# Performance work log

Hardware: AMD Instinct MI355X
Metric: run time of the kernel (lower is better)

The kernel has to match this reference:

```python
import jax, jax.numpy as jnp
import numpy as np

B, T, D = 256, 512, 64
E = 32            # station embedding dim
H = 256           # hidden size
HOR = 24          # horizon steps
STATIONS = 1000
DIN0 = D + E      # effective input dim of layer 0


def _grud_cell(x, mask, delta, x_last, h_prev, gx, gh, Wr, br, Wz, bz, Wh, bh):
    # x, mask, delta, x_last: [B, din]; h_prev: [B, H]
    x_decayed = jnp.exp(-jax.nn.relu(delta * gx)) * x_last
    x_filled = jnp.where(mask > 0, x, x_decayed)
    h_decay = jnp.exp(-jax.nn.relu(delta.mean(axis=1, keepdims=True) * gh))
    h_dec = h_decay * h_prev
    comb = jnp.concatenate([x_filled, h_dec], axis=1)
    r = jax.nn.sigmoid(comb @ Wr + br)
    z = jax.nn.sigmoid(comb @ Wz + bz)
    comb_h = jnp.concatenate([x_filled, r * h_dec], axis=1)
    h_tilde = jnp.tanh(comb_h @ Wh + bh)
    return (1.0 - z) * h_dec + z * h_tilde


def setup_inputs() -> dict:
    key = jax.random.key(0)
    ks = jax.random.split(key, 32)
    def lin(k, fan_in, fan_out):
        bound = 1.0 / np.sqrt(fan_in)
        kw, kb = jax.random.split(k)
        W = jax.random.uniform(kw, (fan_in, fan_out), jnp.float32, -bound, bound)
        b = jax.random.uniform(kb, (fan_out,), jnp.float32, -bound, bound)
        return W, b
    x = jax.random.normal(ks[0], (B, T, D), jnp.float32)
    mask = (jax.random.uniform(ks[1], (B, T, D)) < 0.8).astype(jnp.float32)
    delta = jax.random.uniform(ks[2], (B, T, D), jnp.float32)
    x_last_obs = jax.random.normal(ks[3], (B, T, D), jnp.float32)
    station_idx = jax.random.randint(ks[4], (B,), 0, STATIONS)
    emb = jax.random.normal(ks[5], (STATIONS, E), jnp.float32)
    Wr0, br0 = lin(ks[6], DIN0 + H, H)
    Wz0, bz0 = lin(ks[7], DIN0 + H, H)
    Wh0, bh0 = lin(ks[8], DIN0 + H, H)
    Wr1, br1 = lin(ks[9], H + H, H)
    Wz1, bz1 = lin(ks[10], H + H, H)
    Wh1, bh1 = lin(ks[11], H + H, H)
    Wp1, bp1 = lin(ks[12], H, H)
    Wp2, bp2 = lin(ks[13], H, HOR * 2)
    return dict(x=x, mask=mask, delta=delta, x_last_obs=x_last_obs,
                station_idx=station_idx, emb=emb,
                gx0=jnp.ones((DIN0,), jnp.float32), gh0=jnp.ones((H,), jnp.float32),
                Wr0=Wr0, br0=br0, Wz0=Wz0, bz0=bz0, Wh0=Wh0, bh0=bh0,
                gx1=jnp.ones((H,), jnp.float32), gh1=jnp.ones((H,), jnp.float32),
                Wr1=Wr1, br1=br1, Wz1=Wz1, bz1=bz1, Wh1=Wh1, bh1=bh1,
                Wp1=Wp1, bp1=bp1, Wp2=Wp2, bp2=bp2)


def reference(x, mask, delta, x_last_obs, station_idx, emb,
              gx0, gh0, Wr0, br0, Wz0, bz0, Wh0, bh0,
              gx1, gh1, Wr1, br1, Wz1, bz1, Wh1, bh1,
              Wp1, bp1, Wp2, bp2):
    e = emb[station_idx]                              # [B, E]
    e_seq = jnp.broadcast_to(e[:, None, :], (B, T, E))
    x_c = jnp.concatenate([x, e_seq], axis=-1)        # [B, T, D+E]
    xl_c = jnp.concatenate([x_last_obs, e_seq], axis=-1)
    m_c = jnp.concatenate([mask, jnp.zeros((B, T, E), x.dtype)], axis=-1)
    d_c = jnp.concatenate([delta, jnp.zeros((B, T, E), x.dtype)], axis=-1)
    # wait: torch does NOT extend mask/delta; it keeps them at input_dim? No —
    # cell expects delta shape == input_dim of the cell. In torch, mask/delta are
    # NOT concatenated, which would break shapes unless mask/delta already match.
    # Torch code passes mask[:, t, :] of width D into a cell of width D+E; torch
    # broadcasting of elementwise ops (delta * gamma_x with gamma_x width D+E)
    # would fail unless D == D+E. Faithful runnable semantics: embedding slots are
    # always 'observed' with zero delta (mask=1, delta=0, last_obs=emb).
    m_c = jnp.concatenate([mask, jnp.ones((B, T, E), x.dtype)], axis=-1)

    # time-major for scan: [T, B, *]
    xs = (jnp.swapaxes(x_c, 0, 1), jnp.swapaxes(m_c, 0, 1),
          jnp.swapaxes(d_c, 0, 1), jnp.swapaxes(xl_c, 0, 1))

    ones_h = jnp.ones((B, H), x.dtype)
    zeros_h = jnp.zeros((B, H), x.dtype)

    def step(hs, inp):
        h0, h1 = hs
        x_t, m_t, d_t, xl_t = inp
        h0 = _grud_cell(x_t, m_t, d_t, xl_t, h0, gx0, gh0, Wr0, br0, Wz0, bz0, Wh0, bh0)
        # layer 1: mask=1, delta=0, x_last = h0 (as in torch forward)
        h1 = _grud_cell(h0, ones_h, zeros_h, h0, h1, gx1, gh1, Wr1, br1, Wz1, bz1, Wh1, bh1)
        return (h0, h1), None

    (h0, h1), _ = jax.lax.scan(step, (zeros_h, zeros_h), xs)
    out = jax.nn.relu(h1 @ Wp1 + bp1) @ Wp2 + bp2     # [B, HOR*2]
    return out.reshape(B, HOR, 2)
```

## Files before the change

kernel.cpp:

```cpp
#include <hip/hip_runtime.h>
#include <hip/hip_fp16.h>


#define BB   256
#define TT   512
#define DX   64
#define EE   32
#define HH   256
#define RING 4

#define OFF_W0X_R 0
#define OFF_W0X_Z 24576
#define OFF_W0X_H 49152
#define OFF_W0H_R 73728
#define OFF_W0H_Z 139264
#define OFF_W0H_H 204800
#define OFF_W1X_R 270336
#define OFF_W1X_Z 335872
#define OFF_W1X_H 401408
#define OFF_W1H_R 466944
#define OFF_W1H_Z 532480
#define OFF_W1H_H 598016
#define PACK_TOTAL 663552

#define MSG_OFF   1327104
#define MSG_U32   768
#define FLAG_OFF  (MSG_OFF + 128*RING*MSG_U32*4)
#define CFLAG_OFF (FLAG_OFF + 128*RING*4)

typedef _Float16 half2_t __attribute__((ext_vector_type(2)));

__global__ void pack_weights(const float* __restrict__ Wr0, const float* __restrict__ Wz0,
                             const float* __restrict__ Wh0, const float* __restrict__ Wr1,
                             const float* __restrict__ Wz1, const float* __restrict__ Wh1,
                             __half* __restrict__ dst) {
  int idx = blockIdx.x * blockDim.x + threadIdx.x;
  if (idx >= PACK_TOTAL) return;
  const float* src;
  int row0, local;
  if (idx < 73728) {
    int r = idx / 24576; local = idx % 24576;
    src = (r == 0) ? Wr0 : (r == 1) ? Wz0 : Wh0;
    row0 = 0;
  } else {
    int q = (idx - 73728) / 65536; local = (idx - 73728) % 65536;
    if (q < 3)      { src = (q == 0) ? Wr0 : (q == 1) ? Wz0 : Wh0; row0 = 96;  }
    else if (q < 6) { src = (q == 3) ? Wr1 : (q == 4) ? Wz1 : Wh1; row0 = 0;   }
    else            { src = (q == 6) ? Wr1 : (q == 7) ? Wz1 : Wh1; row0 = 256; }
  }
  int seg = local >> 13;
  int rem = local & 8191;
  int j   = rem >> 5;
  int s   = (rem >> 3) & 3;
  int i   = rem & 7;
  int row = row0 + seg * 32 + s * 8 + i;
  dst[idx] = __float2half(src[(size_t)row * HH + j]);
}

__device__ __forceinline__ float dot8(uint4 w, uint4 v, float acc) {
#if __has_builtin(__builtin_amdgcn_fdot2)
  union { uint4 u; half2_t h[4]; } W, V;
  W.u = w; V.u = v;
  acc = __builtin_amdgcn_fdot2(W.h[0], V.h[0], acc, false);
  acc = __builtin_amdgcn_fdot2(W.h[1], V.h[1], acc, false);
  acc = __builtin_amdgcn_fdot2(W.h[2], V.h[2], acc, false);
  acc = __builtin_amdgcn_fdot2(W.h[3], V.h[3], acc, false);
#else
  union { unsigned u; __half2 h; } cw, cv;
  float2 wf, vf;
  cw.u = w.x; cv.u = v.x; wf = __half22float2(cw.h); vf = __half22float2(cv.h);
  acc = fmaf(wf.x, vf.x, acc); acc = fmaf(wf.y, vf.y, acc);
  cw.u = w.y; cv.u = v.y; wf = __half22float2(cw.h); vf = __half22float2(cv.h);
  acc = fmaf(wf.x, vf.x, acc); acc = fmaf(wf.y, vf.y, acc);
  cw.u = w.z; cv.u = v.z; wf = __half22float2(cw.h); vf = __half22float2(cv.h);
  acc = fmaf(wf.x, vf.x, acc); acc = fmaf(wf.y, vf.y, acc);
  cw.u = w.w; cv.u = v.w; wf = __half22float2(cw.h); vf = __half22float2(cv.h);
  acc = fmaf(wf.x, vf.x, acc); acc = fmaf(wf.y, vf.y, acc);
#endif
  return acc;
}

__device__ __forceinline__ float kred(float a) {
  a += __shfl_xor(a, 1, 64);
  a += __shfl_xor(a, 2, 64);
  return a;
}

__device__ __forceinline__ float sigm(float x) { return 1.f / (1.f + __expf(-x)); }

__device__ __forceinline__ void spin_eq(uint32_t* p, uint32_t want) {
  for (int it = 0; it < 1000000; ++it) {
    if (__hip_atomic_load(p, __ATOMIC_RELAXED, __HIP_MEMORY_SCOPE_AGENT) == want) return;
    __builtin_amdgcn_s_sleep(1);
  }
}

__global__ __launch_bounds__(1024)
__attribute__((amdgpu_waves_per_eu(4, 4)))
void grud_pipe(const float* __restrict__ x, const float* __restrict__ mask,
               const float* __restrict__ delta, const float* __restrict__ xl,
               const int* __restrict__ sidx, const float* __restrict__ emb,
               const float* __restrict__ gx0, const float* __restrict__ gh0,
               const float* __restrict__ br0, const float* __restrict__ bz0,
               const float* __restrict__ bh0, const float* __restrict__ br1,
               const float* __restrict__ bz1, const float* __restrict__ bh1,
               const float* __restrict__ Wp1, const float* __restrict__ bp1,
               const float* __restrict__ Wp2, const float* __restrict__ bp2,
               const __half* __restrict__ PW, uint32_t* wsu, float* __restrict__ out)
{
  const int bid = blockIdx.x;
  const bool isA = bid < 128;
  const int pair = isA ? bid : (bid - 128);
  const int tid = threadIdx.x;
  const int j = tid >> 2, s = tid & 3, s8 = s * 8, jb = j * 4 + s;

  uint32_t* msgbase = wsu + (MSG_OFF >> 2) + (size_t)pair * (RING * MSG_U32);
  uint32_t* flag    = wsu + (FLAG_OFF >> 2) + pair * RING;
  uint32_t* cflag   = wsu + (CFLAG_OFF >> 2) + pair * RING;

  __shared__ __align__(16) uint4  wlds[8192];
  __shared__ __align__(16) __half xfh[2][96];
  __shared__ __align__(16) __half hdech[2][256];
  __shared__ __align__(16) __half rhh[2][256];
  __shared__ __align__(16) __half h0h[2][256];
  __shared__ __align__(16) __half h0c[2][256];
  __shared__ __align__(16) __half h1h[2][256];
  __shared__ __align__(16) float  fbuf[2][256];
  __shared__ float p1f[256];
  __shared__ float sdel[2];

  if (isA) {
    const uint4* W0XR = (const uint4*)(PW + OFF_W0X_R);
    const uint4* W0XZ = (const uint4*)(PW + OFF_W0X_Z);
    const uint4* W0XH = (const uint4*)(PW + OFF_W0X_H);
    const uint4* W0HR = (const uint4*)(PW + OFF_W0H_R);
    const uint4* W0HZ = (const uint4*)(PW + OFF_W0H_Z);
    const uint4* W0HH = (const uint4*)(PW + OFF_W0H_H);
    const uint4* W1XH = (const uint4*)(PW + OFF_W1X_H);
    #pragma unroll 2
    for (int seg = 0; seg < 8; ++seg) wlds[seg * 1024 + jb] = W0HH[seg * 1024 + jb];

    const float brj0 = br0[j], bzj0 = bz0[j], bhj0 = bh0[j];
    const float gh0j = gh0[j];
    float h0j0 = 0.f, h0j1 = 0.f;
    if (tid < 512) { int g = tid >> 8, k = tid & 255; h0h[g][k] = __float2half(0.f); }
    if (tid < 64)  { int g = tid >> 5, e = tid & 31;
                     xfh[g][DX + e] = __float2half(emb[(size_t)sidx[2 * pair + g] * EE + e]); }
    float gx0k = 0.f;
    if (tid < 128) gx0k = gx0[tid & 63];
    const size_t xb0 = (size_t)(2 * pair) * TT * DX, xb1 = (size_t)(2 * pair + 1) * TT * DX;
    float xv = 0, mv = 0, dv = 0, xlv = 0;
    if (tid < 128) { size_t a = (tid < 64 ? xb0 : xb1) + (tid & 63);
                     xv = x[a]; mv = mask[a]; dv = delta[a]; xlv = xl[a]; }
    __syncthreads();

    for (int t = 0; t < TT; ++t) {
      const int slot = t & (RING - 1);
      if (tid == 0 && t >= RING) spin_eq(&cflag[slot], (uint32_t)(t - RING + 1));
      if (tid < 128) {
        int g = tid >> 6;
        float xd = __expf(-fmaxf(dv * gx0k, 0.f)) * xlv;
        xfh[g][tid & 63] = __float2half(mv > 0.f ? xv : xd);
        float ssum = dv;
        #pragma unroll
        for (int o = 32; o > 0; o >>= 1) ssum += __shfl_down(ssum, o, 64);
        if ((tid & 63) == 0) sdel[g] = ssum * (1.f / 96.f);
      }
      __syncthreads();
      float hd0 = __expf(-fmaxf(sdel[0] * gh0j, 0.f)) * h0j0;
      float hd1 = __expf(-fmaxf(sdel[1] * gh0j, 0.f)) * h0j1;
      if (s == 0) { hdech[0][j] = __float2half(hd0); hdech[1][j] = __float2half(hd1); }
      __syncthreads();
      if (tid < 128 && t + 1 < TT) {
        size_t a = (tid < 64 ? xb0 : xb1) + (size_t)(t + 1) * DX + (tid & 63);
        xv = x[a]; mv = mask[a]; dv = delta[a]; xlv = xl[a];
      }
      float ar0 = 0, ar1v = 0, az0 = 0, az1v = 0, ah0 = 0, ah1v = 0;
      #pragma unroll
      for (int seg = 0; seg < 3; ++seg) {
        uint4 v0 = *(const uint4*)(&xfh[0][seg * 32 + s8]);
        uint4 v1 = *(const uint4*)(&xfh[1][seg * 32 + s8]);
        uint4 wr = W0XR[seg * 1024 + jb], wz = W0XZ[seg * 1024 + jb], wh = W0XH[seg * 1024 + jb];
        ar0 = dot8(wr, v0, ar0); ar1v = dot8(wr, v1, ar1v);
        az0 = dot8(wz, v0, az0); az1v = dot8(wz, v1, az1v);
        ah0 = dot8(wh, v0, ah0); ah1v = dot8(wh, v1, ah1v);
      }
      #pragma unroll 2
      for (int seg = 0; seg < 8; ++seg) {
        uint4 v0 = *(const uint4*)(&hdech[0][seg * 32 + s8]);
        uint4 v1 = *(const uint4*)(&hdech[1][seg * 32 + s8]);
        uint4 wr = W0HR[seg * 1024 + jb], wz = W0HZ[seg * 1024 + jb];
        ar0 = dot8(wr, v0, ar0); ar1v = dot8(wr, v1, ar1v);
        az0 = dot8(wz, v0, az0); az1v = dot8(wz, v1, az1v);
      }
      ar0 = kred(ar0) + brj0; ar1v = kred(ar1v) + brj0;
      az0 = kred(az0) + bzj0; az1v = kred(az1v) + bzj0;
      float r0 = sigm(ar0), r1g = sigm(ar1v), z0 = sigm(az0), z1g = sigm(az1v);
      if (s == 0) { rhh[0][j] = __float2half(r0 * hd0); rhh[1][j] = __float2half(r1g * hd1); }
      __syncthreads();
      #pragma unroll 2
      for (int seg = 0; seg < 8; ++seg) {
        uint4 w  = wlds[seg * 1024 + jb];
        uint4 v0 = *(const uint4*)(&rhh[0][seg * 32 + s8]);
        uint4 v1 = *(const uint4*)(&rhh[1][seg * 32 + s8]);
        ah0 = dot8(w, v0, ah0); ah1v = dot8(w, v1, ah1v);
      }
      ah0 = kred(ah0) + bhj0; ah1v = kred(ah1v) + bhj0;
      h0j0 = (1.f - z0) * hd0 + z0 * tanhf(ah0);
      h0j1 = (1.f - z1g) * hd1 + z1g * tanhf(ah1v);
      if (s == 0) { h0h[0][j] = __float2half(h0j0); h0h[1][j] = __float2half(h0j1); }
      __syncthreads();
      float ax0 = 0.f, ax1 = 0.f;
      #pragma unroll 2
      for (int seg = 0; seg < 8; ++seg) {
        uint4 w  = W1XH[seg * 1024 + jb];
        uint4 v0 = *(const uint4*)(&h0h[0][seg * 32 + s8]);
        uint4 v1 = *(const uint4*)(&h0h[1][seg * 32 + s8]);
        ax0 = dot8(w, v0, ax0); ax1 = dot8(w, v1, ax1);
      }
      ax0 = kred(ax0); ax1 = kred(ax1);
      uint32_t* msg = msgbase + slot * MSG_U32;
      if (s == 0) {
        __hip_atomic_store(msg + 256 + j, __float_as_uint(ax0), __ATOMIC_RELAXED, __HIP_MEMORY_SCOPE_AGENT);
        __hip_atomic_store(msg + 512 + j, __float_as_uint(ax1), __ATOMIC_RELAXED, __HIP_MEMORY_SCOPE_AGENT);
      }
      if (tid < 256)
        __hip_atomic_store(msg + tid, ((const uint32_t*)h0h)[tid], __ATOMIC_RELAXED, __HIP_MEMORY_SCOPE_AGENT);
      __syncthreads();
      if (tid == 0)
        __hip_atomic_store(&flag[slot], (uint32_t)(t + 1), __ATOMIC_RELAXED, __HIP_MEMORY_SCOPE_AGENT);
    }
  } else {
    const uint4* W1XR = (const uint4*)(PW + OFF_W1X_R);
    const uint4* W1XZ = (const uint4*)(PW + OFF_W1X_Z);
    const uint4* W1HR = (const uint4*)(PW + OFF_W1H_R);
    const uint4* W1HZ = (const uint4*)(PW + OFF_W1H_Z);
    const uint4* W1HH = (const uint4*)(PW + OFF_W1H_H);
    #pragma unroll 2
    for (int seg = 0; seg < 8; ++seg) wlds[seg * 1024 + jb] = W1HH[seg * 1024 + jb];
    const float brj1 = br1[j], bzj1 = bz1[j], bhj1 = bh1[j];
    float h1j0 = 0.f, h1j1 = 0.f;
    if (tid < 512) { int g = tid >> 8, k = tid & 255; h1h[g][k] = __float2half(0.f); }
    __syncthreads();

    for (int t = 0; t < TT; ++t) {
      const int slot = t & (RING - 1);
      if (tid == 0) spin_eq(&flag[slot], (uint32_t)(t + 1));
      __syncthreads();
      uint32_t* msg = msgbase + slot * MSG_U32;
      if (tid < 256)
        ((uint32_t*)h0c)[tid] = __hip_atomic_load(msg + tid, __ATOMIC_RELAXED, __HIP_MEMORY_SCOPE_AGENT);
      else if (tid < 768) {
        int idx = tid - 256;
        fbuf[idx >> 8][idx & 255] =
            __uint_as_float(__hip_atomic_load(msg + tid, __ATOMIC_RELAXED, __HIP_MEMORY_SCOPE_AGENT));
      }
      __syncthreads();
      if (tid == 0)
        __hip_atomic_store(&cflag[slot], (uint32_t)(t + 1), __ATOMIC_RELAXED, __HIP_MEMORY_SCOPE_AGENT);
      float ar0 = 0, ar1v = 0, az0 = 0, az1v = 0;
      #pragma unroll 2
      for (int seg = 0; seg < 8; ++seg) {
        uint4 u0 = *(const uint4*)(&h0c[0][seg * 32 + s8]);
        uint4 u1 = *(const uint4*)(&h0c[1][seg * 32 + s8]);
        uint4 v0 = *(const uint4*)(&h1h[0][seg * 32 + s8]);
        uint4 v1 = *(const uint4*)(&h1h[1][seg * 32 + s8]);
        uint4 wxr = W1XR[seg * 1024 + jb], wxz = W1XZ[seg * 1024 + jb];
        uint4 whr = W1HR[seg * 1024 + jb], whz = W1HZ[seg * 1024 + jb];
        ar0 = dot8(wxr, u0, ar0);  ar0 = dot8(whr, v0, ar0);
        ar1v = dot8(wxr, u1, ar1v); ar1v = dot8(whr, v1, ar1v);
        az0 = dot8(wxz, u0, az0);  az0 = dot8(whz, v0, az0);
        az1v = dot8(wxz, u1, az1v); az1v = dot8(whz, v1, az1v);
      }
      ar0 = kred(ar0) + brj1; ar1v = kred(ar1v) + brj1;
      az0 = kred(az0) + bzj1; az1v = kred(az1v) + bzj1;
      float r0 = sigm(ar0), r1g = sigm(ar1v), z0 = sigm(az0), z1g = sigm(az1v);
      if (s == 0) { rhh[0][j] = __float2half(r0 * h1j0); rhh[1][j] = __float2half(r1g * h1j1); }
      __syncthreads();
      float p0 = 0.f, p1 = 0.f;
      #pragma unroll 2
      for (int seg = 0; seg < 8; ++seg) {
        uint4 w  = wlds[seg * 1024 + jb];
        uint4 v0 = *(const uint4*)(&rhh[0][seg * 32 + s8]);
        uint4 v1 = *(const uint4*)(&rhh[1][seg * 32 + s8]);
        p0 = dot8(w, v0, p0); p1 = dot8(w, v1, p1);
      }
      p0 = kred(p0); p1 = kred(p1);
      float ahf0 = fbuf[0][j] + p0 + bhj1;
      float ahf1 = fbuf[1][j] + p1 + bhj1;
      h1j0 = (1.f - z0) * h1j0 + z0 * tanhf(ahf0);
      h1j1 = (1.f - z1g) * h1j1 + z1g * tanhf(ahf1);
      if (s == 0) { h1h[0][j] = __float2half(h1j0); h1h[1][j] = __float2half(h1j1); }
    }

    if (s == 0) { fbuf[0][j] = h1j0; fbuf[1][j] = h1j1; }
    __syncthreads();
    for (int g = 0; g < 2; ++g) {
      float a1 = 0.f; int k0 = s * 64;
      #pragma unroll 8
      for (int k = 0; k < 64; ++k) a1 = fmaf(fbuf[g][k0 + k], Wp1[(size_t)(k0 + k) * HH + j], a1);
      a1 = kred(a1) + bp1[j];
      if (s == 0) p1f[j] = fmaxf(a1, 0.f);
      __syncthreads();
      if (tid < 192) {
        int jo = tid >> 2, so = tid & 3; float o = 0.f; int kk0 = so * 64;
        #pragma unroll 8
        for (int k = 0; k < 64; ++k) o = fmaf(p1f[kk0 + k], Wp2[(size_t)(kk0 + k) * 48 + jo], o);
        o += __shfl_xor(o, 1, 64);
        o += __shfl_xor(o, 2, 64);
        if (so == 0) out[(size_t)(2 * pair + g) * 48 + jo] = o + bp2[jo];
      }
      __syncthreads();
    }
  }
}

extern "C" void kernel_launch(void* const* d_in, const int* in_sizes, int n_in,
                              void* d_out, int out_size, void* d_ws, size_t ws_size,
                              hipStream_t stream) {
  const float* x    = (const float*)d_in[0];
  const float* mask = (const float*)d_in[1];
  const float* delta= (const float*)d_in[2];
  const float* xl   = (const float*)d_in[3];
  const int*   sidx = (const int*)d_in[4];
  const float* emb  = (const float*)d_in[5];
  const float* gx0  = (const float*)d_in[6];
  const float* gh0  = (const float*)d_in[7];
  const float* Wr0  = (const float*)d_in[8];
  const float* br0  = (const float*)d_in[9];
  const float* Wz0  = (const float*)d_in[10];
  const float* bz0  = (const float*)d_in[11];
  const float* Wh0  = (const float*)d_in[12];
  const float* bh0  = (const float*)d_in[13];
  const float* Wr1  = (const float*)d_in[16];
  const float* br1  = (const float*)d_in[17];
  const float* Wz1  = (const float*)d_in[18];
  const float* bz1  = (const float*)d_in[19];
  const float* Wh1  = (const float*)d_in[20];
  const float* bh1  = (const float*)d_in[21];
  const float* Wp1  = (const float*)d_in[22];
  const float* bp1  = (const float*)d_in[23];
  const float* Wp2  = (const float*)d_in[24];
  const float* bp2  = (const float*)d_in[25];
  __half*   PW  = (__half*)d_ws;
  uint32_t* wsu = (uint32_t*)d_ws;
  float* out = (float*)d_out;

  hipLaunchKernelGGL(pack_weights, dim3((PACK_TOTAL + 255) / 256), dim3(256), 0, stream,
                     Wr0, Wz0, Wh0, Wr1, Wz1, Wh1, PW);
  hipLaunchKernelGGL(grud_pipe, dim3(BB), dim3(1024), 0, stream,
                     x, mask, delta, xl, sidx, emb, gx0, gh0,
                     br0, bz0, bh0, br1, bz1, bh1, Wp1, bp1, Wp2, bp2, PW, wsu, out);
}
```

Before: 3.593 ms.

## Overlap layer-1 recurrent gate dots with the wait and add fast math

```diff
diff --git a/kernel.cpp b/kernel.cpp
--- a/kernel.cpp
+++ b/kernel.cpp
@@ -86,7 +86,25 @@
   return a;
 }
 
-__device__ __forceinline__ float sigm(float x) { return 1.f / (1.f + __expf(-x)); }
+__device__ __forceinline__ float wsum64(float v) {
+  #pragma unroll
+  for (int o = 32; o > 0; o >>= 1) v += __shfl_xor(v, o, 64);
+  return v;
+}
+
+__device__ __forceinline__ float rcpf(float v) {
+#if __has_builtin(__builtin_amdgcn_rcpf)
+  return __builtin_amdgcn_rcpf(v);
+#else
+  return 1.f / v;
+#endif
+}
+__device__ __forceinline__ float sigm(float v) { return rcpf(1.f + __expf(-v)); }
+__device__ __forceinline__ float tanh_fast(float v) {
+  float t = __expf(-2.f * fabsf(v));
+  float r = (1.f - t) * rcpf(1.f + t);
+  return copysignf(r, v);
+}
 
 __device__ __forceinline__ void spin_eq(uint32_t* p, uint32_t want) {
   for (int it = 0; it < 1000000; ++it) {
@@ -127,7 +145,6 @@
   __shared__ __align__(16) __half h1h[2][256];
   __shared__ __align__(16) float  fbuf[2][256];
   __shared__ float p1f[256];
-  __shared__ float sdel[2];
 
   if (isA) {
     const uint4* W0XR = (const uint4*)(PW + OFF_W0X_R);
@@ -143,7 +160,6 @@
     const float brj0 = br0[j], bzj0 = bz0[j], bhj0 = bh0[j];
     const float gh0j = gh0[j];
     float h0j0 = 0.f, h0j1 = 0.f;
-    if (tid < 512) { int g = tid >> 8, k = tid & 255; h0h[g][k] = __float2half(0.f); }
     if (tid < 64)  { int g = tid >> 5, e = tid & 31;
                      xfh[g][DX + e] = __float2half(emb[(size_t)sidx[2 * pair + g] * EE + e]); }
     float gx0k = 0.f;
@@ -157,33 +173,43 @@
     for (int t = 0; t < TT; ++t) {
       const int slot = t & (RING - 1);
       if (tid == 0 && t >= RING) spin_eq(&cflag[slot], (uint32_t)(t - RING + 1));
+      uint4 a0 = W0XR[jb], a1 = W0XR[1024 + jb], a2 = W0XR[2048 + jb];
+      uint4 a3 = W0XZ[jb], a4 = W0XZ[1024 + jb], a5 = W0XZ[2048 + jb];
+      uint4 a6 = W0XH[jb], a7 = W0XH[1024 + jb], a8 = W0XH[2048 + jb];
       if (tid < 128) {
-        int g = tid >> 6;
         float xd = __expf(-fmaxf(dv * gx0k, 0.f)) * xlv;
-        xfh[g][tid & 63] = __float2half(mv > 0.f ? xv : xd);
-        float ssum = dv;
-        #pragma unroll
-        for (int o = 32; o > 0; o >>= 1) ssum += __shfl_down(ssum, o, 64);
-        if ((tid & 63) == 0) sdel[g] = ssum * (1.f / 96.f);
-      }
-      __syncthreads();
-      float hd0 = __expf(-fmaxf(sdel[0] * gh0j, 0.f)) * h0j0;
-      float hd1 = __expf(-fmaxf(sdel[1] * gh0j, 0.f)) * h0j1;
-      if (s == 0) { hdech[0][j] = __float2half(hd0); hdech[1][j] = __float2half(hd1); }
-      __syncthreads();
+        xfh[tid >> 6][tid & 63] = __float2half(mv > 0.f ? xv : xd);
+      }
+      {
+        size_t dofs = (size_t)t * DX + (tid & 63);
+        float sd0 = wsum64(delta[xb0 + dofs]) * (1.f / 96.f);
+        float sd1 = wsum64(delta[xb1 + dofs]) * (1.f / 96.f);
+        float hd0 = __expf(-fmaxf(sd0 * gh0j, 0.f)) * h0j0;
+        float hd1 = __expf(-fmaxf(sd1 * gh0j, 0.f)) * h0j1;
+        if (s == 0) { hdech[0][j] = __float2half(hd0); hdech[1][j] = __float2half(hd1); }
+        fbuf[0][j] = hd0;
+        fbuf[1][j] = hd1;
+      }
+      __syncthreads();
+      float hd0 = fbuf[0][j], hd1 = fbuf[1][j];
       if (tid < 128 && t + 1 < TT) {
         size_t a = (tid < 64 ? xb0 : xb1) + (size_t)(t + 1) * DX + (tid & 63);
         xv = x[a]; mv = mask[a]; dv = delta[a]; xlv = xl[a];
       }
       float ar0 = 0, ar1v = 0, az0 = 0, az1v = 0, ah0 = 0, ah1v = 0;
-      #pragma unroll
-      for (int seg = 0; seg < 3; ++seg) {
-        uint4 v0 = *(const uint4*)(&xfh[0][seg * 32 + s8]);
-        uint4 v1 = *(const uint4*)(&xfh[1][seg * 32 + s8]);
-        uint4 wr = W0XR[seg * 1024 + jb], wz = W0XZ[seg * 1024 + jb], wh = W0XH[seg * 1024 + jb];
-        ar0 = dot8(wr, v0, ar0); ar1v = dot8(wr, v1, ar1v);
-        az0 = dot8(wz, v0, az0); az1v = dot8(wz, v1, az1v);
-        ah0 = dot8(wh, v0, ah0); ah1v = dot8(wh, v1, ah1v);
+      {
+        uint4 v00 = *(const uint4*)(&xfh[0][s8]);
+        uint4 v01 = *(const uint4*)(&xfh[0][32 + s8]);
+        uint4 v02 = *(const uint4*)(&xfh[0][64 + s8]);
+        uint4 v10 = *(const uint4*)(&xfh[1][s8]);
+        uint4 v11 = *(const uint4*)(&xfh[1][32 + s8]);
+        uint4 v12 = *(const uint4*)(&xfh[1][64 + s8]);
+        ar0 = dot8(a0, v00, ar0); ar0 = dot8(a1, v01, ar0); ar0 = dot8(a2, v02, ar0);
+        ar1v = dot8(a0, v10, ar1v); ar1v = dot8(a1, v11, ar1v); ar1v = dot8(a2, v12, ar1v);
+        az0 = dot8(a3, v00, az0); az0 = dot8(a4, v01, az0); az0 = dot8(a5, v02, az0);
+        az1v = dot8(a3, v10, az1v); az1v = dot8(a4, v11, az1v); az1v = dot8(a5, v12, az1v);
+        ah0 = dot8(a6, v00, ah0); ah0 = dot8(a7, v01, ah0); ah0 = dot8(a8, v02, ah0);
+        ah1v = dot8(a6, v10, ah1v); ah1v = dot8(a7, v11, ah1v); ah1v = dot8(a8, v12, ah1v);
       }
       #pragma unroll 2
       for (int seg = 0; seg < 8; ++seg) {
@@ -206,8 +232,8 @@
         ah0 = dot8(w, v0, ah0); ah1v = dot8(w, v1, ah1v);
       }
       ah0 = kred(ah0) + bhj0; ah1v = kred(ah1v) + bhj0;
-      h0j0 = (1.f - z0) * hd0 + z0 * tanhf(ah0);
-      h0j1 = (1.f - z1g) * hd1 + z1g * tanhf(ah1v);
+      h0j0 = (1.f - z0) * hd0 + z0 * tanh_fast(ah0);
+      h0j1 = (1.f - z1g) * hd1 + z1g * tanh_fast(ah1v);
       if (s == 0) { h0h[0][j] = __float2half(h0j0); h0h[1][j] = __float2half(h0j1); }
       __syncthreads();
       float ax0 = 0.f, ax1 = 0.f;
@@ -241,10 +267,19 @@
     const float brj1 = br1[j], bzj1 = bz1[j], bhj1 = bh1[j];
     float h1j0 = 0.f, h1j1 = 0.f;
     if (tid < 512) { int g = tid >> 8, k = tid & 255; h1h[g][k] = __float2half(0.f); }
-    __syncthreads();
 
     for (int t = 0; t < TT; ++t) {
       const int slot = t & (RING - 1);
+      __syncthreads();
+      float ar0 = 0, ar1v = 0, az0 = 0, az1v = 0;
+      #pragma unroll 2
+      for (int seg = 0; seg < 8; ++seg) {
+        uint4 v0 = *(const uint4*)(&h1h[0][seg * 32 + s8]);
+        uint4 v1 = *(const uint4*)(&h1h[1][seg * 32 + s8]);
+        uint4 whr = W1HR[seg * 1024 + jb], whz = W1HZ[seg * 1024 + jb];
+        ar0 = dot8(whr, v0, ar0); ar1v = dot8(whr, v1, ar1v);
+        az0 = dot8(whz, v0, az0); az1v = dot8(whz, v1, az1v);
+      }
       if (tid == 0) spin_eq(&flag[slot], (uint32_t)(t + 1));
       __syncthreads();
       uint32_t* msg = msgbase + slot * MSG_U32;
@@ -258,19 +293,13 @@
       __syncthreads();
       if (tid == 0)
         __hip_atomic_store(&cflag[slot], (uint32_t)(t + 1), __ATOMIC_RELAXED, __HIP_MEMORY_SCOPE_AGENT);
-      float ar0 = 0, ar1v = 0, az0 = 0, az1v = 0;
       #pragma unroll 2
       for (int seg = 0; seg < 8; ++seg) {
         uint4 u0 = *(const uint4*)(&h0c[0][seg * 32 + s8]);
         uint4 u1 = *(const uint4*)(&h0c[1][seg * 32 + s8]);
-        uint4 v0 = *(const uint4*)(&h1h[0][seg * 32 + s8]);
-        uint4 v1 = *(const uint4*)(&h1h[1][seg * 32 + s8]);
         uint4 wxr = W1XR[seg * 1024 + jb], wxz = W1XZ[seg * 1024 + jb];
-        uint4 whr = W1HR[seg * 1024 + jb], whz = W1HZ[seg * 1024 + jb];
-        ar0 = dot8(wxr, u0, ar0);  ar0 = dot8(whr, v0, ar0);
-        ar1v = dot8(wxr, u1, ar1v); ar1v = dot8(whr, v1, ar1v);
-        az0 = dot8(wxz, u0, az0);  az0 = dot8(whz, v0, az0);
-        az1v = dot8(wxz, u1, az1v); az1v = dot8(whz, v1, az1v);
+        ar0 = dot8(wxr, u0, ar0); ar1v = dot8(wxr, u1, ar1v);
+        az0 = dot8(wxz, u0, az0); az1v = dot8(wxz, u1, az1v);
       }
       ar0 = kred(ar0) + brj1; ar1v = kred(ar1v) + brj1;
       az0 = kred(az0) + bzj1; az1v = kred(az1v) + bzj1;
@@ -288,11 +317,12 @@
       p0 = kred(p0); p1 = kred(p1);
       float ahf0 = fbuf[0][j] + p0 + bhj1;
       float ahf1 = fbuf[1][j] + p1 + bhj1;
-      h1j0 = (1.f - z0) * h1j0 + z0 * tanhf(ahf0);
-      h1j1 = (1.f - z1g) * h1j1 + z1g * tanhf(ahf1);
+      h1j0 = (1.f - z0) * h1j0 + z0 * tanh_fast(ahf0);
+      h1j1 = (1.f - z1g) * h1j1 + z1g * tanh_fast(ahf1);
       if (s == 0) { h1h[0][j] = __float2half(h1j0); h1h[1][j] = __float2half(h1j1); }
     }
 
+    __syncthreads();
     if (s == 0) { fbuf[0][j] = h1j0; fbuf[1][j] = h1j1; }
     __syncthreads();
     for (int g = 0; g < 2; ++g) {
```

After: 3.492 ms. 1.03x faster.
